# Kernel optimization log

Hardware: AMD Instinct MI355X
Metric: run time of the kernel (lower is better)

Reference implementation:

```python
import jax, jax.numpy as jnp
import numpy as np

B, S, LEN = 1024, 64, 48          # batch, max atoms, atoms per molecule
N = B * LEN                        # total nodes = node_mask.sum()
E = 4 * N                          # edges (avg degree ~4)
D = 256                            # input_dim == hidden_dim == d_model == d_ff
H, HD = D // 8, 8                  # num_heads = hidden_dim // 8
L = 3                              # transformer layers
VOCAB = 65


def _ln(z, s, b):
    mu = z.mean(-1, keepdims=True)
    var = ((z - mu) ** 2).mean(-1, keepdims=True)
    return (z - mu) * jax.lax.rsqrt(var + 1e-5) * s + b


def _forward(x_atoms, edge_index, node_mask, emb_table, conv1_w, conv1_b,
             conv2_w, conv2_b, in_w, in_b, attn_w, attn_b, proj_w, proj_b,
             ln1_s, ln1_b, ff1_w, ff1_b, ff2_w, ff2_b, ln2_s, ln2_b):
    n = x_atoms.shape[0]
    src, dst = edge_index[0], edge_index[1]
    # Embedding with max_norm=1 (torch renormalizes accessed rows)
    e = emb_table[x_atoms]
    nrm = jnp.linalg.norm(e, axis=-1, keepdims=True)
    e = e * jnp.minimum(1.0, 1.0 / (nrm + 1e-7))
    # GCN symmetric normalization with self-loops (shared by both convs)
    deg = jax.ops.segment_sum(jnp.ones((src.shape[0],), e.dtype), dst, num_segments=n) + 1.0
    dinv = jax.lax.rsqrt(deg)
    coef = (dinv[src] * dinv[dst])[:, None]       # per-edge norm
    self_coef = (dinv * dinv)[:, None]            # self-loop norm

    def gcn(h, W, b):
        h = h @ W
        agg = jax.ops.segment_sum(h[src] * coef, dst, num_segments=n)
        return agg + h * self_coef + b

    ones = jnp.ones((n, 1), e.dtype)
    pe = jax.nn.relu(gcn(ones, conv1_w, conv1_b))
    pe = gcn(pe, conv2_w, conv2_b)
    x = e + pe
    # masked_scatter into padded [B, S, D] (row-major fill order)
    mflat = node_mask.reshape(-1)
    rank = jnp.clip(jnp.cumsum(mflat) - 1, 0, n - 1)
    padded = jnp.where(mflat[:, None], x[rank], 0.0).reshape(B, S, D)
    # transformer encoder, post-LN, ReLU FFN; mask [B,1,S,1] as in original
    h = padded @ in_w + in_b
    qmask = node_mask[:, None, :, None]
    scale = 1.0 / np.sqrt(HD).astype(np.float32)
    for l in range(L):
        qkv = h @ attn_w[l] + attn_b[l]
        q, k, v = jnp.split(qkv, 3, axis=-1)
        q = q.reshape(B, S, H, HD)
        k = k.reshape(B, S, H, HD)
        v = v.reshape(B, S, H, HD)
        scores = jnp.einsum('bqhd,bkhd->bhqk', q, k) * scale
        scores = jnp.where(qmask, scores, -1e9)
        attn = jax.nn.softmax(scores, axis=-1)
        o = jnp.einsum('bhqk,bkhd->bqhd', attn, v).reshape(B, S, D)
        h = _ln(h + o @ proj_w[l] + proj_b[l], ln1_s[l], ln1_b[l])
        ff = jax.nn.relu(h @ ff1_w[l] + ff1_b[l]) @ ff2_w[l] + ff2_b[l]
        h = _ln(h + ff, ln2_s[l], ln2_b[l])
    return h


def setup_inputs() -> dict:
    key = jax.random.key(0)
    ks = jax.random.split(key, 16)
    x_atoms = jax.random.randint(ks[0], (N,), 0, VOCAB)
    edge_index = jax.random.randint(ks[1], (2, E), 0, N)
    node_mask = jnp.broadcast_to(jnp.arange(S)[None, :] < LEN, (B, S))
    f32 = jnp.float32
    p = lambda k, shp: (jax.random.normal(k, shp, f32) * 0.02)
    return {
        'x_atoms': x_atoms, 'edge_index': edge_index, 'node_mask': node_mask,
        'emb_table': jax.random.normal(ks[2], (VOCAB, D), f32),
        'conv1_w': p(ks[3], (1, D)), 'conv1_b': jnp.zeros((D,), f32),
        'conv2_w': p(ks[4], (D, D)), 'conv2_b': jnp.zeros((D,), f32),
        'in_w': p(ks[5], (D, D)), 'in_b': jnp.zeros((D,), f32),
        'attn_w': p(ks[6], (L, D, 3 * D)), 'attn_b': jnp.zeros((L, 3 * D), f32),
        'proj_w': p(ks[7], (L, D, D)), 'proj_b': jnp.zeros((L, D), f32),
        'ln1_s': jnp.ones((L, D), f32), 'ln1_b': jnp.zeros((L, D), f32),
        'ff1_w': p(ks[8], (L, D, D)), 'ff1_b': jnp.zeros((L, D), f32),
        'ff2_w': p(ks[9], (L, D, D)), 'ff2_b': jnp.zeros((L, D), f32),
        'ln2_s': jnp.ones((L, D), f32), 'ln2_b': jnp.zeros((L, D), f32),
    }


def reference(x_atoms, edge_index, node_mask, emb_table, conv1_w, conv1_b,
              conv2_w, conv2_b, in_w, in_b, attn_w, attn_b, proj_w, proj_b,
              ln1_s, ln1_b, ff1_w, ff1_b, ff2_w, ff2_b, ln2_s, ln2_b):
    return _forward(x_atoms, edge_index, node_mask, emb_table, conv1_w, conv1_b,
                    conv2_w, conv2_b, in_w, in_b, attn_w, attn_b, proj_w, proj_b,
                    ln1_s, ln1_b, ff1_w, ff1_b, ff2_w, ff2_b, ln2_s, ln2_b)
```

## Files before the change

kernel.cpp:

```cpp
#include <hip/hip_runtime.h>
#include <cstdint>
#include <cstddef>

#define B_   1024
#define S_   64
#define LEN_ 48
#define NN   (B_*LEN_)
#define EE   (4*NN)
#define D_   256
#define H_   32
#define HD_  8
#define ROWS (B_*S_)
#define PLANE 16777216

typedef float  f32x4  __attribute__((ext_vector_type(4)));
typedef __bf16 bf16x8 __attribute__((ext_vector_type(8)));

#define AS1(p) ((const __attribute__((address_space(1))) void*)(p))
#define AS3(p) ((__attribute__((address_space(3))) void*)(p))

__device__ __forceinline__ unsigned short f2bf(float f) {
    union { float f; unsigned u; } x; x.f = f;
    unsigned r = x.u + 0x7fffu + ((x.u >> 16) & 1u);
    return (unsigned short)(r >> 16);
}
__device__ __forceinline__ float bf2f(unsigned short h) {
    union { unsigned u; float f; } x; x.u = (unsigned)h << 16; return x.f;
}
__device__ __forceinline__ bf16x8 u4_to_bf8(uint4 u) {
    union { uint4 u; bf16x8 v; } c; c.u = u; return c.v;
}

__global__ void embed_kernel(const int* __restrict__ atoms,
                             const float* __restrict__ table,
                             float* __restrict__ e) {
    int wave = threadIdx.x >> 6, lane = threadIdx.x & 63;
    int row  = blockIdx.x * 4 + wave;
    int a    = atoms[row];
    float4 v = ((const float4*)(table + (size_t)a * D_))[lane];
    float ss = v.x*v.x + v.y*v.y + v.z*v.z + v.w*v.w;
    #pragma unroll
    for (int off = 32; off; off >>= 1) ss += __shfl_xor(ss, off);
    float nrm = sqrtf(ss);
    float sc  = fminf(1.0f, 1.0f / (nrm + 1e-7f));
    v.x *= sc; v.y *= sc; v.z *= sc; v.w *= sc;
    ((float4*)(e + (size_t)row * D_))[lane] = v;
}

__global__ void fill_kernel(const int* __restrict__ ei, int* __restrict__ cur,
                            int* __restrict__ bucket) {
    int e = blockIdx.x * 256 + threadIdx.x;
    if (e < EE) {
        int s = ei[e], d = ei[EE + e];
        int pos = atomicAdd(&cur[d], 1);
        if (pos < 32) bucket[d * 32 + pos] = s;
    }
}

__global__ void dinv_kernel(const int* __restrict__ cur, float* __restrict__ dinv) {
    int i = blockIdx.x * 256 + threadIdx.x;
    if (i < NN) dinv[i] = rsqrtf((float)cur[i] + 1.0f);
}

__global__ void agg1_kernel(const int* __restrict__ ei, const float* __restrict__ dinv,
                            float* __restrict__ agg1) {
    int e = blockIdx.x * 256 + threadIdx.x;
    if (e < EE) {
        int s = ei[e], d = ei[EE + e];
        atomicAdd(&agg1[d], dinv[s] * dinv[d]);
    }
}

__global__ void pe1_kernel(const float* __restrict__ agg1, const float* __restrict__ dinv,
                           const float* __restrict__ w1, const float* __restrict__ b1,
                           unsigned short* __restrict__ pe1) {
    size_t idx = (size_t)blockIdx.x * 256 + threadIdx.x;
    int i = (int)(idx >> 8), d = (int)(idx & 255);
    float c = agg1[i] + dinv[i] * dinv[i];
    pe1[idx] = f2bf(fmaxf(0.0f, w1[d] * c + b1[d]));
}

__global__ void wconv_kernel(const float* __restrict__ conv2_w, const float* __restrict__ in_w,
                             const float* __restrict__ attn_w, const float* __restrict__ proj_w,
                             const float* __restrict__ ff1_w, const float* __restrict__ ff2_w,
                             unsigned short* __restrict__ wt) {
    int z = blockIdx.y;
    int n = blockIdx.x, k = threadIdx.x;
    const float* src; unsigned short* dst; int N = 256;
    if      (z == 0) { src = conv2_w;                       dst = wt; }
    else if (z == 1) { src = in_w;                          dst = wt + 65536; }
    else if (z <  5) { int l = z - 2;  src = attn_w + (size_t)l * 196608; dst = wt + 131072  + (size_t)l * 196608; N = 768; }
    else if (z <  8) { int l = z - 5;  src = proj_w + (size_t)l * 65536;  dst = wt + 720896  + (size_t)l * 65536; }
    else if (z < 11) { int l = z - 8;  src = ff1_w  + (size_t)l * 65536;  dst = wt + 917504  + (size_t)l * 65536; }
    else             { int l = z - 11; src = ff2_w  + (size_t)l * 65536;  dst = wt + 1114112 + (size_t)l * 65536; }
    if (n < N) dst[(size_t)n * 256 + k] = f2bf(src[(size_t)k * N + n]);
}

__global__ __launch_bounds__(256) void gemm2(
        const unsigned short* __restrict__ A, const unsigned short* __restrict__ WT,
        const float* __restrict__ bias, unsigned short* __restrict__ C0,
        float* __restrict__ Cf, const unsigned short* __restrict__ zeros,
        int mt, int amode, int cmode, int relu) {
    __shared__ unsigned short sh[16384];
    unsigned short* Asm = sh;
    unsigned short* Wsm = sh + 8192;
    const int t = threadIdx.x, w = t >> 6, lane = t & 63;
    const int lr = lane & 15, lq = lane >> 4;
    const int nt = gridDim.x / mt;
    const int xcd = blockIdx.x & 7;
    const int sb  = blockIdx.x >> 3;
    const int bx = sb % nt;
    const int by = (sb / nt) * 8 + xcd;
    const size_t m0 = (size_t)by * 128;
    const int    n0 = bx * 128;
    const int    N  = nt * 128;
    const int    wr = (w >> 1) * 64, wc = (w & 1) * 64;

    f32x4 acc[4][4];
    #pragma unroll
    for (int mi = 0; mi < 4; mi++)
        #pragma unroll
        for (int tt = 0; tt < 4; tt++) acc[mi][tt] = (f32x4){0.f, 0.f, 0.f, 0.f};

    const int srow = w * 32 + (lane >> 3);
    const int sj   = lane & 7;

    for (int ki = 0; ki < 4; ki++) {
        if (ki) __syncthreads();
        #pragma unroll
        for (int c = 0; c < 4; c++) {
            int row = srow + c * 8;
            {
                int gch = sj ^ (row & 7);
                const unsigned short* g;
                if (amode == 0) {
                    g = A + (m0 + row) * 256 + ki * 64 + gch * 8;
                } else {
                    size_t grow = m0 + row;
                    int s = (int)(grow & 63);
                    g = (s < LEN_) ? (A + ((grow >> 6) * LEN_ + s) * 256 + ki * 64 + gch * 8)
                                   : zeros;
                }
                __builtin_amdgcn_global_load_lds(AS1(g), AS3(Asm + w * 2048 + c * 512), 16, 0, 0);
            }
            {
                int gch = sj ^ (row & 7);
                const unsigned short* g = WT + (size_t)(n0 + row) * 256 + ki * 64 + gch * 8;
                __builtin_amdgcn_global_load_lds(AS1(g), AS3(Wsm + w * 2048 + c * 512), 16, 0, 0);
            }
        }
        __syncthreads();
        #pragma unroll
        for (int ks = 0; ks < 2; ks++) {
            bf16x8 af[4], bfr[4];
            #pragma unroll
            for (int mi = 0; mi < 4; mi++) {
                int row = wr + mi * 16 + lr;
                int cs = (ks * 4 + lq) ^ (row & 7);
                af[mi] = *(const bf16x8*)&Asm[row * 64 + cs * 8];
            }
            #pragma unroll
            for (int tt = 0; tt < 4; tt++) {
                int col = wc + tt * 16 + lr;
                int cs = (ks * 4 + lq) ^ (col & 7);
                bfr[tt] = *(const bf16x8*)&Wsm[col * 64 + cs * 8];
            }
            #pragma unroll
            for (int mi = 0; mi < 4; mi++)
                #pragma unroll
                for (int tt = 0; tt < 4; tt++)
                    acc[mi][tt] = __builtin_amdgcn_mfma_f32_16x16x32_bf16(af[mi], bfr[tt], acc[mi][tt], 0, 0, 0);
        }
    }
    if (cmode == 2) {
        #pragma unroll
        for (int tt = 0; tt < 4; tt++) {
            int c = n0 + wc + tt * 16 + lr;
            float bv = bias ? bias[c] : 0.0f;
            #pragma unroll
            for (int mi = 0; mi < 4; mi++)
                #pragma unroll
                for (int r = 0; r < 4; r++) {
                    size_t grow = m0 + wr + mi * 16 + lq * 4 + r;
                    float v = acc[mi][tt][r] + bv;
                    C0[grow * 256 + c] = f2bf(v);
                    Cf[grow * 256 + c] = v;
                }
        }
    } else {
        __syncthreads();
        #pragma unroll
        for (int tt = 0; tt < 4; tt++) {
            int col = wc + tt * 16 + lr;
            float bv = bias ? bias[n0 + col] : 0.0f;
            #pragma unroll
            for (int mi = 0; mi < 4; mi++)
                #pragma unroll
                for (int r = 0; r < 4; r++) {
                    int row = wr + mi * 16 + lq * 4 + r;
                    float v = acc[mi][tt][r] + bv;
                    if (relu) v = fmaxf(v, 0.0f);
                    sh[row * 128 + (((col >> 3) ^ (row & 15)) << 3) + (col & 7)] = f2bf(v);
                }
        }
        __syncthreads();
        #pragma unroll
        for (int i = 0; i < 8; i++) {
            int id = i * 256 + t;
            int row = id >> 4, hch = id & 15;
            uint4 val = *(const uint4*)&sh[row * 128 + ((hch ^ (row & 15)) << 3)];
            size_t grow = m0 + row;
            int c0 = n0 + hch * 8;
            if (cmode == 0) {
                *(uint4*)&C0[grow * (size_t)N + c0] = val;
            } else {
                int p = c0 >> 8, h = (c0 >> 3) & 31;
                *(uint4*)&C0[(size_t)p * PLANE + ((grow >> 6) * 32 + h) * 512 + (grow & 63) * 8] = val;
            }
        }
    }
}

__global__ void gather_kernel(const float* __restrict__ xbuf, const unsigned short* __restrict__ h2,
                              const int* __restrict__ cur, const int* __restrict__ bucket,
                              const float* __restrict__ dinv, const float* __restrict__ b2,
                              unsigned short* __restrict__ xg) {
    int w = threadIdx.x >> 6, lane = threadIdx.x & 63;
    int i = blockIdx.x * 4 + w;
    float di = dinv[i];
    ushort4 hv = ((const ushort4*)(h2 + (size_t)i * D_))[lane];
    float4  xv = ((const float4*)(xbuf + (size_t)i * D_))[lane];
    float4  bv = ((const float4*)b2)[lane];
    float a0 = xv.x + bf2f(hv.x) * di * di + bv.x;
    float a1 = xv.y + bf2f(hv.y) * di * di + bv.y;
    float a2 = xv.z + bf2f(hv.z) * di * di + bv.z;
    float a3 = xv.w + bf2f(hv.w) * di * di + bv.w;
    int deg = min(cur[i], 32);
    for (int e = 0; e < deg; e++) {
        int s = bucket[i * 32 + e];
        float c = dinv[s] * di;
        ushort4 sv = ((const ushort4*)(h2 + (size_t)s * D_))[lane];
        a0 += bf2f(sv.x) * c;
        a1 += bf2f(sv.y) * c;
        a2 += bf2f(sv.z) * c;
        a3 += bf2f(sv.w) * c;
    }
    ushort4 out;
    out.x = f2bf(a0); out.y = f2bf(a1); out.z = f2bf(a2); out.w = f2bf(a3);
    ((ushort4*)(xg + (size_t)i * D_))[lane] = out;
}

__global__ __launch_bounds__(256) void attn3_kernel(unsigned short* __restrict__ qkv) {
    __shared__ unsigned short Pb[4][64 * 64];
    __shared__ unsigned short VTb[4][16 * 64];
    const int b = blockIdx.x;
    const int w = threadIdx.x >> 6, lane = threadIdx.x & 63;
    const int lr = lane & 15, lq = lane >> 4;
    unsigned short* Pw  = Pb[w];
    unsigned short* VTw = VTb[w];
    const uint4* Q4 = (const uint4*)qkv;
    const uint4* K4 = Q4 + PLANE / 8;
    const uint4* V4 = Q4 + 2 * (PLANE / 8);
    unsigned short* o = qkv;
    const float scale = 0.35355339059327373f;
    const bf16x8 zf = u4_to_bf8(make_uint4(0, 0, 0, 0));

    for (int hh = 0; hh < 8; hh++) {
        const int h = w * 8 + hh;
        const size_t hb = ((size_t)b * 32 + h) * 64;

        {
            uint4 vrow = V4[hb + lane];
            union { uint4 u; unsigned short s[8]; } vu; vu.u = vrow;
            int ch = lane >> 3, jj = lane & 7;
            #pragma unroll
            for (int d = 0; d < 8; d++)
                VTw[d * 64 + (ch ^ (d & 7)) * 8 + jj] = vu.s[d];
        }

        bf16x8 af[4], bfk[4];
        #pragma unroll
        for (int mi = 0; mi < 4; mi++)
            af[mi] = (lq == 0) ? u4_to_bf8(Q4[hb + mi * 16 + lr]) : zf;
        #pragma unroll
        for (int ni = 0; ni < 4; ni++)
            bfk[ni] = (lq == 0) ? u4_to_bf8(K4[hb + ni * 16 + lr]) : zf;
        f32x4 s[4][4];
        #pragma unroll
        for (int mi = 0; mi < 4; mi++)
            #pragma unroll
            for (int ni = 0; ni < 4; ni++)
                s[mi][ni] = __builtin_amdgcn_mfma_f32_16x16x32_bf16(
                    af[mi], bfk[ni], (f32x4){0.f, 0.f, 0.f, 0.f}, 0, 0, 0);
        #pragma unroll
        for (int ni = 0; ni < 4; ni++) s[3][ni] = (f32x4){0.f, 0.f, 0.f, 0.f};

        #pragma unroll
        for (int mi = 0; mi < 4; mi++) {
            float mx[4], sm[4];
            #pragma unroll
            for (int r = 0; r < 4; r++)
                mx[r] = fmaxf(fmaxf(s[mi][0][r], s[mi][1][r]), fmaxf(s[mi][2][r], s[mi][3][r]));
            #pragma unroll
            for (int st = 1; st <= 8; st <<= 1)
                #pragma unroll
                for (int r = 0; r < 4; r++) mx[r] = fmaxf(mx[r], __shfl_xor(mx[r], st));
            #pragma unroll
            for (int ni = 0; ni < 4; ni++)
                #pragma unroll
                for (int r = 0; r < 4; r++)
                    s[mi][ni][r] = __expf((s[mi][ni][r] - mx[r]) * scale);
            #pragma unroll
            for (int r = 0; r < 4; r++)
                sm[r] = (s[mi][0][r] + s[mi][1][r]) + (s[mi][2][r] + s[mi][3][r]);
            #pragma unroll
            for (int st = 1; st <= 8; st <<= 1)
                #pragma unroll
                for (int r = 0; r < 4; r++) sm[r] += __shfl_xor(sm[r], st);
            #pragma unroll
            for (int r = 0; r < 4; r++) sm[r] = 1.0f / sm[r];
            #pragma unroll
            for (int ni = 0; ni < 4; ni++) {
                int ch = ni * 2 + (lr >> 3), jj = lr & 7;
                #pragma unroll
                for (int r = 0; r < 4; r++) {
                    int q = mi * 16 + lq * 4 + r;
                    Pw[q * 64 + (ch ^ (q & 7)) * 8 + jj] = f2bf(s[mi][ni][r] * sm[r]);
                }
            }
        }

        bf16x8 av[2];
        #pragma unroll
        for (int ks = 0; ks < 2; ks++) {
            int cs = (ks * 4 + lq) ^ (lr & 7);
            av[ks] = *(const bf16x8*)&VTw[lr * 64 + cs * 8];
        }
        #pragma unroll
        for (int ni = 0; ni < 4; ni++) {
            f32x4 oa = (f32x4){0.f, 0.f, 0.f, 0.f};
            #pragma unroll
            for (int ks = 0; ks < 2; ks++) {
                int q = ni * 16 + lr;
                int cs = (ks * 4 + lq) ^ (q & 7);
                bf16x8 pb = *(const bf16x8*)&Pw[q * 64 + cs * 8];
                oa = __builtin_amdgcn_mfma_f32_16x16x32_bf16(av[ks], pb, oa, 0, 0, 0);
            }
            if (lq < 2) {
                int q = ni * 16 + lr;
                ushort4 ov;
                ov.x = f2bf(oa[0]); ov.y = f2bf(oa[1]);
                ov.z = f2bf(oa[2]); ov.w = f2bf(oa[3]);
                *(ushort4*)(o + (hb + q) * 8 + lq * 4) = ov;
            }
        }
    }
}

__global__ __launch_bounds__(256) void projln_kernel(
        const unsigned short* __restrict__ A, const unsigned short* __restrict__ WT,
        const float* __restrict__ bias, const float* __restrict__ resid,
        const float* __restrict__ g, const float* __restrict__ bb,
        float* __restrict__ outF, unsigned short* __restrict__ outB, int aplane) {
    __shared__ unsigned short Asm[64 * 64];
    __shared__ unsigned short Wsm[256 * 64];
    const int t = threadIdx.x, w = t >> 6, lane = t & 63;
    const int lr = lane & 15, lq = lane >> 4;
    const size_t m0 = (size_t)blockIdx.x * 64;
    f32x4 acc[16];
    #pragma unroll
    for (int tt = 0; tt < 16; tt++) acc[tt] = (f32x4){0.f, 0.f, 0.f, 0.f};

    for (int ki = 0; ki < 4; ki++) {
        if (ki) __syncthreads();
        #pragma unroll
        for (int c = 0; c < 2; c++) {
            int rowl = w * 16 + (lane >> 3) + c * 8;
            int gch = (lane & 7) ^ (rowl & 7);
            const unsigned short* gsrc = aplane
                ? A + (((size_t)blockIdx.x * 32 + ki * 8 + gch) * 64 + rowl) * 8
                : A + (m0 + rowl) * 256 + ki * 64 + gch * 8;
            __builtin_amdgcn_global_load_lds(AS1(gsrc), AS3(Asm + w * 1024 + c * 512), 16, 0, 0);
        }
        #pragma unroll
        for (int c = 0; c < 8; c++) {
            int row = w * 64 + (lane >> 3) + c * 8;
            const unsigned short* gsrc = WT + (size_t)row * 256 + ki * 64 + ((lane & 7) ^ (row & 7)) * 8;
            __builtin_amdgcn_global_load_lds(AS1(gsrc), AS3(Wsm + w * 4096 + c * 512), 16, 0, 0);
        }
        __syncthreads();
        #pragma unroll
        for (int ks = 0; ks < 2; ks++) {
            int cs = ((ks * 4 + lq) ^ (lr & 7)) << 3;
            int ra = w * 16 + lr;
            bf16x8 af = *(const bf16x8*)&Asm[ra * 64 + cs];
            #pragma unroll
            for (int tt = 0; tt < 16; tt++) {
                int col = tt * 16 + lr;
                bf16x8 bfr = *(const bf16x8*)&Wsm[col * 64 + cs];
                acc[tt] = __builtin_amdgcn_mfma_f32_16x16x32_bf16(af, bfr, acc[tt], 0, 0, 0);
            }
        }
    }
    float s1[4] = {0.f,0.f,0.f,0.f}, s2[4] = {0.f,0.f,0.f,0.f};
    #pragma unroll
    for (int tt = 0; tt < 16; tt++) {
        int col = tt * 16 + lr;
        float bv = bias[col];
        #pragma unroll
        for (int r = 0; r < 4; r++) {
            size_t grow = m0 + w * 16 + lq * 4 + r;
            float z = acc[tt][r] + bv + resid[grow * 256 + col];
            acc[tt][r] = z;
            s1[r] += z; s2[r] += z * z;
        }
    }
    #pragma unroll
    for (int st = 1; st <= 8; st <<= 1)
        #pragma unroll
        for (int r = 0; r < 4; r++) { s1[r] += __shfl_xor(s1[r], st); s2[r] += __shfl_xor(s2[r], st); }
    float mu[4], rs[4];
    #pragma unroll
    for (int r = 0; r < 4; r++) {
        mu[r] = s1[r] * (1.0f / 256.0f);
        float var = s2[r] * (1.0f / 256.0f) - mu[r] * mu[r];
        rs[r] = rsqrtf(var + 1e-5f);
    }
    #pragma unroll
    for (int tt = 0; tt < 16; tt++) {
        int col = tt * 16 + lr;
        float gv = g[col], bv2 = bb[col];
        #pragma unroll
        for (int r = 0; r < 4; r++) {
            size_t grow = m0 + w * 16 + lq * 4 + r;
            float v = (acc[tt][r] - mu[r]) * rs[r] * gv + bv2;
            outF[grow * 256 + col] = v;
            outB[grow * 256 + col] = f2bf(v);
        }
    }
}

__global__ __launch_bounds__(256) void ffn_kernel(
        const unsigned short* __restrict__ A,
        const unsigned short* __restrict__ W1T, const float* __restrict__ b1,
        const unsigned short* __restrict__ W2T, const float* __restrict__ b2,
        const float* __restrict__ resid,
        const float* __restrict__ g, const float* __restrict__ bb,
        float* __restrict__ outF, unsigned short* __restrict__ outB) {
    __shared__ unsigned short Wsm[256 * 64];
    __shared__ unsigned short T[64 * 256];
    const int t = threadIdx.x, w = t >> 6, lane = t & 63;
    const int lr = lane & 15, lq = lane >> 4;
    const size_t m0 = (size_t)blockIdx.x * 64;

    uint4 afu[8];
    {
        const unsigned short* arow = A + (m0 + w * 16 + lr) * 256 + lq * 8;
        #pragma unroll
        for (int s = 0; s < 8; s++) afu[s] = *(const uint4*)(arow + s * 32);
    }
    f32x4 acc[16];
    #pragma unroll
    for (int tt = 0; tt < 16; tt++) acc[tt] = (f32x4){0.f, 0.f, 0.f, 0.f};

    for (int ki = 0; ki < 4; ki++) {
        if (ki) __syncthreads();
        #pragma unroll
        for (int i = 0; i < 8; i++) {
            int id = i * 256 + t;
            int row = id >> 3, c = id & 7;
            const unsigned short* src = W1T + (size_t)row * 256 + ki * 64 + ((c ^ (row & 7)) << 3);
            __builtin_amdgcn_global_load_lds(AS1(src), AS3(Wsm + id * 8), 16, 0, 0);
        }
        __syncthreads();
        #pragma unroll
        for (int ks = 0; ks < 2; ks++) {
            bf16x8 af = u4_to_bf8(afu[ki * 2 + ks]);
            #pragma unroll
            for (int tt = 0; tt < 16; tt++) {
                int row = tt * 16 + lr;
                int pos = (ks * 4 + lq) ^ (row & 7);
                bf16x8 bfr = *(const bf16x8*)&Wsm[row * 64 + pos * 8];
                acc[tt] = __builtin_amdgcn_mfma_f32_16x16x32_bf16(af, bfr, acc[tt], 0, 0, 0);
            }
        }
    }
    #pragma unroll
    for (int tt = 0; tt < 16; tt++) {
        int ff = tt * 16 + lr;
        float bv = b1[ff];
        int chunk = ff >> 3, jj = ff & 7;
        #pragma unroll
        for (int r = 0; r < 4; r++) {
            int m = w * 16 + lq * 4 + r;
            float v = fmaxf(acc[tt][r] + bv, 0.0f);
            int pos = chunk ^ (m & 7) ^ ((m >> 3) & 3);
            T[m * 256 + pos * 8 + jj] = f2bf(v);
            acc[tt][r] = 0.0f;
        }
    }
    for (int ki = 0; ki < 4; ki++) {
        __syncthreads();
        #pragma unroll
        for (int i = 0; i < 8; i++) {
            int id = i * 256 + t;
            int row = id >> 3, c = id & 7;
            const unsigned short* src = W2T + (size_t)row * 256 + ki * 64 + ((c ^ (row & 7)) << 3);
            __builtin_amdgcn_global_load_lds(AS1(src), AS3(Wsm + id * 8), 16, 0, 0);
        }
        __syncthreads();
        #pragma unroll
        for (int ks = 0; ks < 2; ks++) {
            int m = w * 16 + lr;
            int chunk = (ki * 2 + ks) * 4 + lq;
            int pos = chunk ^ (m & 7) ^ ((m >> 3) & 3);
            bf16x8 af = *(const bf16x8*)&T[m * 256 + pos * 8];
            #pragma unroll
            for (int tt = 0; tt < 16; tt++) {
                int row = tt * 16 + lr;
                int wpos = (ks * 4 + lq) ^ (row & 7);
                bf16x8 bfr = *(const bf16x8*)&Wsm[row * 64 + wpos * 8];
                acc[tt] = __builtin_amdgcn_mfma_f32_16x16x32_bf16(af, bfr, acc[tt], 0, 0, 0);
            }
        }
    }
    float s1[4] = {0.f,0.f,0.f,0.f}, s2[4] = {0.f,0.f,0.f,0.f};
    #pragma unroll
    for (int tt = 0; tt < 16; tt++) {
        int col = tt * 16 + lr;
        float bv = b2[col];
        #pragma unroll
        for (int r = 0; r < 4; r++) {
            size_t grow = m0 + w * 16 + lq * 4 + r;
            float z = acc[tt][r] + bv + resid[grow * 256 + col];
            acc[tt][r] = z;
            s1[r] += z; s2[r] += z * z;
        }
    }
    #pragma unroll
    for (int st = 1; st <= 8; st <<= 1)
        #pragma unroll
        for (int r = 0; r < 4; r++) { s1[r] += __shfl_xor(s1[r], st); s2[r] += __shfl_xor(s2[r], st); }
    float mu[4], rs[4];
    #pragma unroll
    for (int r = 0; r < 4; r++) {
        mu[r] = s1[r] * (1.0f / 256.0f);
        float var = s2[r] * (1.0f / 256.0f) - mu[r] * mu[r];
        rs[r] = rsqrtf(var + 1e-5f);
    }
    #pragma unroll
    for (int tt = 0; tt < 16; tt++) {
        int col = tt * 16 + lr;
        float gv = g[col], bv2 = bb[col];
        #pragma unroll
        for (int r = 0; r < 4; r++) {
            size_t grow = m0 + w * 16 + lq * 4 + r;
            float v = (acc[tt][r] - mu[r]) * rs[r] * gv + bv2;
            outF[grow * 256 + col] = v;
            if (outB) outB[grow * 256 + col] = f2bf(v);
        }
    }
}

extern "C" void kernel_launch(void* const* d_in, const int* in_sizes, int n_in,
                              void* d_out, int out_size, void* d_ws, size_t ws_size,
                              hipStream_t stream) {
    const int*   x_atoms = (const int*)d_in[0];
    const int*   ei      = (const int*)d_in[1];
    const float* emb     = (const float*)d_in[3];
    const float* conv1_w = (const float*)d_in[4];
    const float* conv1_b = (const float*)d_in[5];
    const float* conv2_w = (const float*)d_in[6];
    const float* conv2_b = (const float*)d_in[7];
    const float* in_w    = (const float*)d_in[8];
    const float* in_b    = (const float*)d_in[9];
    const float* attn_w  = (const float*)d_in[10];
    const float* attn_b  = (const float*)d_in[11];
    const float* proj_w  = (const float*)d_in[12];
    const float* proj_b  = (const float*)d_in[13];
    const float* ln1_s   = (const float*)d_in[14];
    const float* ln1_b   = (const float*)d_in[15];
    const float* ff1_w   = (const float*)d_in[16];
    const float* ff1_b   = (const float*)d_in[17];
    const float* ff2_w   = (const float*)d_in[18];
    const float* ff2_b   = (const float*)d_in[19];
    const float* ln2_s   = (const float*)d_in[20];
    const float* ln2_b   = (const float*)d_in[21];

    char* ws = (char*)d_ws;
    float*          xbuf = (float*)         (ws + 0);
    unsigned short* pe1  = (unsigned short*)(ws + 50331648);
    unsigned short* xg   = (unsigned short*)(ws + 50331648);
    unsigned short* h2   = (unsigned short*)(ws + 75497472);
    unsigned short* Qp   = (unsigned short*)(ws + 0);
    float*          hbuf = (float*)         (ws + 100663296);
    unsigned short* hbf  = (unsigned short*)(ws + 167772160);
    int*            bucket=(int*)           (ws + 201326592);
    unsigned short* wt   = (unsigned short*)(ws + 207618048);
    int*            cur  = (int*)           (ws + 210239488);
    float*          dinv = (float*)         (ws + 210436096);
    float*          agg1 = (float*)         (ws + 210632704);
    unsigned short* zpage= (unsigned short*)(ws + 210829312);

    hipMemsetAsync(cur,   0, NN * 4, stream);
    hipMemsetAsync(agg1,  0, NN * 4, stream);
    hipMemsetAsync(zpage, 0, 256, stream);

    wconv_kernel<<<dim3(768, 14), 256, 0, stream>>>(conv2_w, in_w, attn_w, proj_w, ff1_w, ff2_w, wt);

    embed_kernel<<<NN / 4, 256, 0, stream>>>(x_atoms, emb, xbuf);
    fill_kernel<<<EE / 256, 256, 0, stream>>>(ei, cur, bucket);
    dinv_kernel<<<NN / 256, 256, 0, stream>>>(cur, dinv);
    agg1_kernel<<<EE / 256, 256, 0, stream>>>(ei, dinv, agg1);
    pe1_kernel<<<NN, 256, 0, stream>>>(agg1, dinv, conv1_w, conv1_b, pe1);
    gemm2<<<768, 256, 0, stream>>>(pe1, wt, nullptr, h2, nullptr, zpage, 384, 0, 0, 0);
    gather_kernel<<<NN / 4, 256, 0, stream>>>(xbuf, h2, cur, bucket, dinv, conv2_b, xg);

    gemm2<<<1024, 256, 0, stream>>>(xg, wt + 65536, in_b, hbf, hbuf, zpage, 512, 1, 2, 0);

    for (int l = 0; l < 3; l++) {
        gemm2<<<3072, 256, 0, stream>>>(
            hbf, wt + 131072 + (size_t)l * 196608, attn_b + (size_t)l * 768,
            Qp, nullptr, zpage, 512, 0, 3, 0);
        attn3_kernel<<<B_, 256, 0, stream>>>(Qp);
        projln_kernel<<<ROWS / 64, 256, 0, stream>>>(
            Qp, wt + 720896 + (size_t)l * 65536, proj_b + (size_t)l * D_, hbuf,
            ln1_s + (size_t)l * D_, ln1_b + (size_t)l * D_, hbuf, hbf, 1);
        ffn_kernel<<<ROWS / 64, 256, 0, stream>>>(
            hbf, wt + 917504 + (size_t)l * 65536, ff1_b + (size_t)l * D_,
            wt + 1114112 + (size_t)l * 65536, ff2_b + (size_t)l * D_, hbuf,
            ln2_s + (size_t)l * D_, ln2_b + (size_t)l * D_,
            (l == 2) ? (float*)d_out : hbuf, (l == 2) ? nullptr : hbf);
    }
}
```

Baseline: 1.001 ms.

## Read GEMM weights directly from global memory instead of staging in LDS

In the projection+LayerNorm and FFN kernels, weight tiles are no longer copied into shared memory with global_load_lds and barriers. Each lane now loads its B fragments straight from global/L2 memory, and the projection kernel also preloads its A fragments into registers. This removes the per-k-step barriers and LDS staging and frees LDS for higher occupancy. The cost is repeated, redundant weight reads across waves going through the cache, with more register pressure and exposed load latency.

```diff
diff --git a/kernel.cpp b/kernel.cpp
--- a/kernel.cpp
+++ b/kernel.cpp
@@ -362,46 +362,39 @@
         const float* __restrict__ bias, const float* __restrict__ resid,
         const float* __restrict__ g, const float* __restrict__ bb,
         float* __restrict__ outF, unsigned short* __restrict__ outB, int aplane) {
-    __shared__ unsigned short Asm[64 * 64];
-    __shared__ unsigned short Wsm[256 * 64];
     const int t = threadIdx.x, w = t >> 6, lane = t & 63;
     const int lr = lane & 15, lq = lane >> 4;
     const size_t m0 = (size_t)blockIdx.x * 64;
+    const int s = w * 16 + lr;
+
+    uint4 afu[8];
+    if (aplane) {
+        #pragma unroll
+        for (int j = 0; j < 8; j++)
+            afu[j] = *(const uint4*)(A + (((size_t)blockIdx.x * 32 + j * 4 + lq) * 64 + s) * 8);
+    } else {
+        const unsigned short* ar = A + (m0 + s) * 256 + lq * 8;
+        #pragma unroll
+        for (int j = 0; j < 8; j++) afu[j] = *(const uint4*)(ar + j * 32);
+    }
+
     f32x4 acc[16];
     #pragma unroll
     for (int tt = 0; tt < 16; tt++) acc[tt] = (f32x4){0.f, 0.f, 0.f, 0.f};
 
-    for (int ki = 0; ki < 4; ki++) {
-        if (ki) __syncthreads();
-        #pragma unroll
-        for (int c = 0; c < 2; c++) {
-            int rowl = w * 16 + (lane >> 3) + c * 8;
-            int gch = (lane & 7) ^ (rowl & 7);
-            const unsigned short* gsrc = aplane
-                ? A + (((size_t)blockIdx.x * 32 + ki * 8 + gch) * 64 + rowl) * 8
-                : A + (m0 + rowl) * 256 + ki * 64 + gch * 8;
-            __builtin_amdgcn_global_load_lds(AS1(gsrc), AS3(Asm + w * 1024 + c * 512), 16, 0, 0);
-        }
-        #pragma unroll
-        for (int c = 0; c < 8; c++) {
-            int row = w * 64 + (lane >> 3) + c * 8;
-            const unsigned short* gsrc = WT + (size_t)row * 256 + ki * 64 + ((lane & 7) ^ (row & 7)) * 8;
-            __builtin_amdgcn_global_load_lds(AS1(gsrc), AS3(Wsm + w * 4096 + c * 512), 16, 0, 0);
-        }
-        __syncthreads();
+    #pragma unroll
+    for (int ki = 0; ki < 4; ki++)
         #pragma unroll
         for (int ks = 0; ks < 2; ks++) {
-            int cs = ((ks * 4 + lq) ^ (lr & 7)) << 3;
-            int ra = w * 16 + lr;
-            bf16x8 af = *(const bf16x8*)&Asm[ra * 64 + cs];
+            bf16x8 af = u4_to_bf8(afu[ki * 2 + ks]);
             #pragma unroll
             for (int tt = 0; tt < 16; tt++) {
                 int col = tt * 16 + lr;
-                bf16x8 bfr = *(const bf16x8*)&Wsm[col * 64 + cs];
+                bf16x8 bfr = *(const bf16x8*)(WT + (size_t)col * 256 + ki * 64 + (ks * 4 + lq) * 8);
                 acc[tt] = __builtin_amdgcn_mfma_f32_16x16x32_bf16(af, bfr, acc[tt], 0, 0, 0);
             }
         }
-    }
+
     float s1[4] = {0.f,0.f,0.f,0.f}, s2[4] = {0.f,0.f,0.f,0.f};
     #pragma unroll
     for (int tt = 0; tt < 16; tt++) {
@@ -447,7 +440,6 @@
         const float* __restrict__ resid,
         const float* __restrict__ g, const float* __restrict__ bb,
         float* __restrict__ outF, unsigned short* __restrict__ outB) {
-    __shared__ unsigned short Wsm[256 * 64];
     __shared__ unsigned short T[64 * 256];
     const int t = threadIdx.x, w = t >> 6, lane = t & 63;
     const int lr = lane & 15, lq = lane >> 4;
@@ -463,28 +455,18 @@
     #pragma unroll
     for (int tt = 0; tt < 16; tt++) acc[tt] = (f32x4){0.f, 0.f, 0.f, 0.f};
 
-    for (int ki = 0; ki < 4; ki++) {
-        if (ki) __syncthreads();
-        #pragma unroll
-        for (int i = 0; i < 8; i++) {
-            int id = i * 256 + t;
-            int row = id >> 3, c = id & 7;
-            const unsigned short* src = W1T + (size_t)row * 256 + ki * 64 + ((c ^ (row & 7)) << 3);
-            __builtin_amdgcn_global_load_lds(AS1(src), AS3(Wsm + id * 8), 16, 0, 0);
-        }
-        __syncthreads();
+    #pragma unroll
+    for (int ki = 0; ki < 4; ki++)
         #pragma unroll
         for (int ks = 0; ks < 2; ks++) {
             bf16x8 af = u4_to_bf8(afu[ki * 2 + ks]);
             #pragma unroll
             for (int tt = 0; tt < 16; tt++) {
                 int row = tt * 16 + lr;
-                int pos = (ks * 4 + lq) ^ (row & 7);
-                bf16x8 bfr = *(const bf16x8*)&Wsm[row * 64 + pos * 8];
+                bf16x8 bfr = *(const bf16x8*)(W1T + (size_t)row * 256 + ki * 64 + (ks * 4 + lq) * 8);
                 acc[tt] = __builtin_amdgcn_mfma_f32_16x16x32_bf16(af, bfr, acc[tt], 0, 0, 0);
             }
         }
-    }
     #pragma unroll
     for (int tt = 0; tt < 16; tt++) {
         int ff = tt * 16 + lr;
@@ -499,16 +481,8 @@
             acc[tt][r] = 0.0f;
         }
     }
-    for (int ki = 0; ki < 4; ki++) {
-        __syncthreads();
-        #pragma unroll
-        for (int i = 0; i < 8; i++) {
-            int id = i * 256 + t;
-            int row = id >> 3, c = id & 7;
-            const unsigned short* src = W2T + (size_t)row * 256 + ki * 64 + ((c ^ (row & 7)) << 3);
-            __builtin_amdgcn_global_load_lds(AS1(src), AS3(Wsm + id * 8), 16, 0, 0);
-        }
-        __syncthreads();
+    #pragma unroll
+    for (int ki = 0; ki < 4; ki++)
         #pragma unroll
         for (int ks = 0; ks < 2; ks++) {
             int m = w * 16 + lr;
@@ -518,12 +492,10 @@
             #pragma unroll
             for (int tt = 0; tt < 16; tt++) {
                 int row = tt * 16 + lr;
-                int wpos = (ks * 4 + lq) ^ (row & 7);
-                bf16x8 bfr = *(const bf16x8*)&Wsm[row * 64 + wpos * 8];
+                bf16x8 bfr = *(const bf16x8*)(W2T + (size_t)row * 256 + ki * 64 + (ks * 4 + lq) * 8);
                 acc[tt] = __builtin_amdgcn_mfma_f32_16x16x32_bf16(af, bfr, acc[tt], 0, 0, 0);
             }
         }
-    }
     float s1[4] = {0.f,0.f,0.f,0.f}, s2[4] = {0.f,0.f,0.f,0.f};
     #pragma unroll
     for (int tt = 0; tt < 16; tt++) {
```

Result: slower. 1.343 ms (+34.2%).
